# Performance work log

Hardware: AMD Instinct MI355X
Metric: run time of the kernel (lower is better)

The kernel has to match this reference:

```python
import jax, jax.numpy as jnp
import numpy as np

EMBED_DIM = 768
HIDDEN_DIM = 384          # max(embed_dim // 2, 128)
NUM_HEADS = 12
HEAD_DIM = EMBED_DIM // NUM_HEADS
LAYER_VOCAB = 4           # len(target_layers)
THRESHOLD = 0.5
MIN_KEEP_RATIO = 0.1
B, N = 8, 1024


def setup_inputs() -> dict:
    key = jax.random.key(0)
    ks = jax.random.split(key, 12)
    std = 0.02
    return {
        "tokens": jax.random.normal(ks[0], (B, N, EMBED_DIM), jnp.float32),
        "layer_token_idx": 1,
        # actor params
        "layer_emb": jax.random.normal(ks[1], (LAYER_VOCAB, EMBED_DIM), jnp.float32) * std,
        "ln_g": jnp.ones((EMBED_DIM,), jnp.float32),
        "ln_b": jnp.zeros((EMBED_DIM,), jnp.float32),
        "w1": jax.random.normal(ks[2], (HIDDEN_DIM, EMBED_DIM), jnp.float32) * std,
        "b1": jnp.zeros((HIDDEN_DIM,), jnp.float32),
        "w2": jax.random.normal(ks[3], (HIDDEN_DIM, HIDDEN_DIM), jnp.float32) * std,
        "b2": jnp.zeros((HIDDEN_DIM,), jnp.float32),
        "w3": jax.random.normal(ks[4], (1, HIDDEN_DIM), jnp.float32) * std,
        "b3": jnp.zeros((1,), jnp.float32),
        # attention params (timm-style)
        "qkv_w": jax.random.normal(ks[5], (3 * EMBED_DIM, EMBED_DIM), jnp.float32) * std,
        "qkv_b": jnp.zeros((3 * EMBED_DIM,), jnp.float32),
        "proj_w": jax.random.normal(ks[6], (EMBED_DIM, EMBED_DIM), jnp.float32) * std,
        "proj_b": jnp.zeros((EMBED_DIM,), jnp.float32),
    }


def _layernorm(x, g, b, eps=1e-5):
    mu = x.mean(-1, keepdims=True)
    var = ((x - mu) ** 2).mean(-1, keepdims=True)
    return (x - mu) * jax.lax.rsqrt(var + eps) * g + b


def _forward(tokens, layer_token_idx, layer_emb, ln_g, ln_b, w1, b1, w2, b2, w3, b3,
             qkv_w, qkv_b, proj_w, proj_b):
    Bsz, Ntok, C = tokens.shape
    # --- MAPPOActor: logits ---
    ctx = tokens + layer_emb[layer_token_idx]               # broadcast [C]
    ctx = ctx + ctx.mean(axis=1, keepdims=True)             # global context
    h = _layernorm(ctx, ln_g, ln_b)
    h = jax.nn.gelu(h @ w1.T + b1, approximate=False)
    h = jax.nn.gelu(h @ w2.T + b2, approximate=False)
    logits = (h @ w3.T + b3).squeeze(-1)                    # [B, N]
    probs = jax.nn.sigmoid(logits)
    # --- compute_mask: threshold + min-keep topk correction ---
    binary = probs >= THRESHOLD                             # [B, N] bool
    min_keep = max(int(Ntok * MIN_KEEP_RATIO), 1)
    min_keep = min(min_keep, Ntok)
    _, topk_idx = jax.lax.top_k(probs, min_keep)            # [B, min_keep]
    fixed = jnp.zeros((Bsz, Ntok), bool).at[jnp.arange(Bsz)[:, None], topk_idx].set(True)
    need_fix = binary.sum(-1) < min_keep                    # [B]
    mask = jnp.where(need_fix[:, None], fixed, binary)
    mask = mask.at[:, 0].set(True)
    # --- masked attention (timm style) ---
    qkv = tokens @ qkv_w.T + qkv_b                          # [B, N, 3C]
    qkv = qkv.reshape(Bsz, Ntok, 3, NUM_HEADS, HEAD_DIM).transpose(2, 0, 3, 1, 4)
    q, k, v = qkv[0], qkv[1], qkv[2]                        # [B, H, N, D]
    q = q * (HEAD_DIM ** -0.5)
    scores = jnp.einsum("bhnd,bhmd->bhnm", q, k)            # [B, H, N, N]
    neg = jnp.finfo(scores.dtype).min
    scores = jnp.where(mask[:, None, None, :], scores, neg)
    attn = jax.nn.softmax(scores, axis=-1)
    v = v * mask[:, None, :, None].astype(v.dtype)
    out = jnp.einsum("bhnm,bhmd->bhnd", attn, v)
    out = out.transpose(0, 2, 1, 3).reshape(Bsz, Ntok, C)
    out = out @ proj_w.T + proj_b
    out = out * mask[..., None].astype(out.dtype)           # zero_out_queries=True
    return out


def reference(tokens, layer_token_idx, layer_emb, ln_g, ln_b, w1, b1, w2, b2, w3, b3,
              qkv_w, qkv_b, proj_w, proj_b):
    return _forward(tokens, layer_token_idx, layer_emb, ln_g, ln_b, w1, b1, w2, b2,
                    w3, b3, qkv_w, qkv_b, proj_w, proj_b)
```

## Files before the change

kernel.cpp:

```cpp
#include <hip/hip_runtime.h>
#include <cstdint>
#include <cmath>

#define EMBED 768
#define HID 384
#define NHEAD 12
#define HDIM 64
#define BATCH 8
#define NTOK 1024
#define MINKEEP 102

using f32x4  = __attribute__((ext_vector_type(4))) float;
using short8 = __attribute__((ext_vector_type(8))) short;
using short4v = __attribute__((ext_vector_type(4))) short;
using half8  = __attribute__((ext_vector_type(8))) _Float16;

__device__ inline short f2bf(float f) {
  unsigned u = __float_as_uint(f);
  u += 0x7fffu + ((u >> 16) & 1u);
  return (short)(u >> 16);
}
__device__ inline float bf2f(short s) {
  return __uint_as_float(((unsigned)(unsigned short)s) << 16);
}
__device__ inline unsigned pack_bf2(float lo, float hi) {
  unsigned ul = __float_as_uint(lo);
  ul += 0x7fffu + ((ul >> 16) & 1u);
  unsigned uh = __float_as_uint(hi);
  uh += 0x7fffu + ((uh >> 16) & 1u);
  return (ul >> 16) | (uh & 0xffff0000u);
}
__device__ inline void split2h(float v, short& h, short& m) {
  _Float16 h0 = (_Float16)v;
  float r = v - (float)h0;
  _Float16 m0 = (_Float16)r;
  h = __builtin_bit_cast(short, h0);
  m = __builtin_bit_cast(short, m0);
}

__global__ __launch_bounds__(768) void addvec_init_kernel(
    const float* __restrict__ layer_emb, const int* __restrict__ lidx,
    float* __restrict__ addvec) {
  int b = blockIdx.x, c = threadIdx.x;
  addvec[b * EMBED + c] = 2.0f * layer_emb[lidx[0] * EMBED + c];
}

__global__ __launch_bounds__(768) void colmean_kernel(
    const float* __restrict__ tokens, float* __restrict__ addvec) {
  int b = blockIdx.x, chunk = blockIdx.y, c = threadIdx.x;
  const float* tb = tokens + ((size_t)b * NTOK + chunk * 64) * EMBED + c;
  float s = 0.f;
#pragma unroll 8
  for (int n = 0; n < 64; ++n) s += tb[(size_t)n * EMBED];
  atomicAdd(&addvec[b * EMBED + c], s * (1.0f / NTOK));
}

__global__ __launch_bounds__(256) void ln_split_kernel(
    const float* __restrict__ tokens, const float* __restrict__ addvec,
    const float* __restrict__ gamma, const float* __restrict__ beta,
    short* __restrict__ xh, short* __restrict__ xm) {
  int row = blockIdx.x;
  int b = row >> 10;
  __shared__ float s_row[EMBED];
  __shared__ float s_red[4];
  const float* tr = tokens + (size_t)row * EMBED;
  const float* av = addvec + b * EMBED;
  float lsum = 0.f;
  for (int c = threadIdx.x; c < EMBED; c += 256) {
    float v = tr[c] + av[c];
    s_row[c] = v;
    lsum += v;
  }
  for (int o = 32; o; o >>= 1) lsum += __shfl_down(lsum, o, 64);
  int wid = threadIdx.x >> 6;
  if ((threadIdx.x & 63) == 0) s_red[wid] = lsum;
  __syncthreads();
  float mu = (s_red[0] + s_red[1] + s_red[2] + s_red[3]) * (1.f / EMBED);
  float lss = 0.f;
  for (int c = threadIdx.x; c < EMBED; c += 256) {
    float d = s_row[c] - mu;
    lss += d * d;
  }
  for (int o = 32; o; o >>= 1) lss += __shfl_down(lss, o, 64);
  __syncthreads();
  if ((threadIdx.x & 63) == 0) s_red[wid] = lss;
  __syncthreads();
  float var = (s_red[0] + s_red[1] + s_red[2] + s_red[3]) * (1.f / EMBED);
  float rinv = 1.0f / sqrtf(var + 1e-5f);
  for (int c = threadIdx.x; c < EMBED; c += 256) {
    float v = (s_row[c] - mu) * rinv * gamma[c] + beta[c];
    short h, m;
    split2h(v, h, m);
    size_t idx = (size_t)row * EMBED + c;
    xh[idx] = h; xm[idx] = m;
  }
}

__global__ __launch_bounds__(256) void cvt_split2_kernel(
    const float* __restrict__ in, short* __restrict__ oh,
    short* __restrict__ om, int n4) {
  int i = blockIdx.x * 256 + threadIdx.x;
  if (i >= n4) return;
  float4 f = ((const float4*)in)[i];
  short4v h, m;
  short th, tm;
  split2h(f.x, th, tm); h[0] = th; m[0] = tm;
  split2h(f.y, th, tm); h[1] = th; m[1] = tm;
  split2h(f.z, th, tm); h[2] = th; m[2] = tm;
  split2h(f.w, th, tm); h[3] = th; m[3] = tm;
  ((short4v*)oh)[i] = h;
  ((short4v*)om)[i] = m;
}

__device__ inline float gelu_exact(float x) {
  return 0.5f * x * (1.0f + erff(x * 0.70710678118654752f));
}

template <int OUT>
__global__ __launch_bounds__(256) void gemm_split_kernel(
    const short* __restrict__ Ah, const short* __restrict__ Am,
    const short* __restrict__ Wh, const short* __restrict__ Wm,
    const float* __restrict__ bias, short* __restrict__ Ch,
    short* __restrict__ Cm, float* __restrict__ Cf,
    int M, int N, int K) {
  __shared__ short sA[2][64][40];
  __shared__ short sW[2][64][40];
  int tid = threadIdx.x;
  int w = tid >> 6, l = tid & 63, lg = l >> 4, lb = l & 15;
  int wr = (w >> 1) * 32, wc = (w & 1) * 32;
  int row0 = blockIdx.x * 64, col0 = blockIdx.y * 64;
  int srow = tid >> 2;
  int skk = (tid & 3) * 8;
  f32x4 acc0[2][2] = {}, acc1[2][2] = {};
  short8 ra0, ra1, rw0, rw1;
  {
    size_t aoff = (size_t)(row0 + srow) * K + skk;
    size_t woff = (size_t)(col0 + srow) * K + skk;
    ra0 = *(const short8*)(Ah + aoff);
    ra1 = *(const short8*)(Am + aoff);
    rw0 = *(const short8*)(Wh + woff);
    rw1 = *(const short8*)(Wm + woff);
  }
  for (int k0 = 0; k0 < K; k0 += 32) {
    __syncthreads();
    *(short8*)&sA[0][srow][skk] = ra0;
    *(short8*)&sA[1][srow][skk] = ra1;
    *(short8*)&sW[0][srow][skk] = rw0;
    *(short8*)&sW[1][srow][skk] = rw1;
    __syncthreads();
    if (k0 + 32 < K) {
      size_t aoff = (size_t)(row0 + srow) * K + k0 + 32 + skk;
      size_t woff = (size_t)(col0 + srow) * K + k0 + 32 + skk;
      ra0 = *(const short8*)(Ah + aoff);
      ra1 = *(const short8*)(Am + aoff);
      rw0 = *(const short8*)(Wh + woff);
      rw1 = *(const short8*)(Wm + woff);
    }
    half8 ah[2], am[2], bh[2], bm[2];
#pragma unroll
    for (int i = 0; i < 2; ++i) {
      ah[i] = *(half8*)&sA[0][wr + i * 16 + lb][lg * 8];
      am[i] = *(half8*)&sA[1][wr + i * 16 + lb][lg * 8];
      bh[i] = *(half8*)&sW[0][wc + i * 16 + lb][lg * 8];
      bm[i] = *(half8*)&sW[1][wc + i * 16 + lb][lg * 8];
    }
#pragma unroll
    for (int i = 0; i < 2; ++i)
#pragma unroll
      for (int j = 0; j < 2; ++j) {
        f32x4 c0 = acc0[i][j];
        f32x4 c1 = acc1[i][j];
        c0 = __builtin_amdgcn_mfma_f32_16x16x32_f16(ah[i], bh[j], c0, 0, 0, 0);
        c1 = __builtin_amdgcn_mfma_f32_16x16x32_f16(ah[i], bm[j], c1, 0, 0, 0);
        c0 = __builtin_amdgcn_mfma_f32_16x16x32_f16(am[i], bh[j], c0, 0, 0, 0);
        acc0[i][j] = c0;
        acc1[i][j] = c1;
      }
  }
#pragma unroll
  for (int i = 0; i < 2; ++i) {
#pragma unroll
    for (int j = 0; j < 2; ++j) {
#pragma unroll
      for (int r = 0; r < 4; ++r) {
        int grow = row0 + wr + i * 16 + lg * 4 + r;
        int gcol = col0 + wc + j * 16 + lb;
        float g = gelu_exact(acc0[i][j][r] + acc1[i][j][r] + bias[gcol]);
        size_t idx = (size_t)grow * N + gcol;
        if (OUT == 0) {
          short h, m;
          split2h(g, h, m);
          Ch[idx] = h; Cm[idx] = m;
        } else {
          Cf[idx] = g;
        }
      }
    }
  }
}

__global__ __launch_bounds__(256) void logits_kernel(
    const float* __restrict__ h2, const float* __restrict__ w3,
    const float* __restrict__ b3, float* __restrict__ probs) {
  int row = blockIdx.x * 4 + (threadIdx.x >> 6);
  int lane = threadIdx.x & 63;
  const float* hr = h2 + (size_t)row * HID;
  float s = 0.f;
  for (int c = lane; c < HID; c += 64) s += hr[c] * w3[c];
  for (int o = 32; o; o >>= 1) s += __shfl_down(s, o, 64);
  if (lane == 0) probs[row] = 1.0f / (1.0f + expf(-(s + b3[0])));
}

__global__ __launch_bounds__(1024) void mask_kernel(
    const float* __restrict__ probs, int* __restrict__ kidx,
    int* __restrict__ kc, float* __restrict__ biasc) {
  int b = blockIdx.x, tid = threadIdx.x;
  __shared__ unsigned long long keys[1024];
  __shared__ int flag[1024];
  __shared__ int wsum[16];
  float p = probs[b * NTOK + tid];
  bool bin = (p >= 0.5f);
  int wid = tid >> 6, lane = tid & 63;
  unsigned long long bal = __ballot(bin);
  if (lane == 0) wsum[wid] = __popcll(bal);
  __syncthreads();
  int total = 0;
  for (int q = 0; q < 16; ++q) total += wsum[q];
  int mv;
  if (total >= MINKEEP) {
    mv = bin ? 1 : 0;
  } else {
    flag[tid] = 0;
    unsigned u = __float_as_uint(p);
    keys[tid] = ((unsigned long long)u << 32) | (unsigned)(1023 - tid);
    __syncthreads();
    for (int k2 = 2; k2 <= 1024; k2 <<= 1) {
      for (int j = k2 >> 1; j > 0; j >>= 1) {
        int ixj = tid ^ j;
        if (ixj > tid) {
          unsigned long long a = keys[tid], c = keys[ixj];
          bool desc = ((tid & k2) == 0);
          if (desc ? (a < c) : (a > c)) {
            keys[tid] = c;
            keys[ixj] = a;
          }
        }
        __syncthreads();
      }
    }
    if (tid < MINKEEP) {
      int idx = 1023 - (int)(keys[tid] & 0xFFFFFFFFu);
      flag[idx] = 1;
    }
    __syncthreads();
    mv = flag[tid];
  }
  if (tid == 0) mv = 1;
  __syncthreads();
  unsigned long long fb = __ballot(mv != 0);
  if (lane == 0) wsum[wid] = __popcll(fb);
  __syncthreads();
  int base = 0, tot = 0;
  for (int q = 0; q < 16; ++q) {
    int v = wsum[q];
    if (q < wid) base += v;
    tot += v;
  }
  int pre = base + __popcll(fb & ((1ull << lane) - 1ull));
  if (mv) {
    kidx[b * NTOK + pre] = tid;
    biasc[b * NTOK + pre] = 0.f;
  }
  if (tid >= tot) {
    kidx[b * NTOK + tid] = 0;
    biasc[b * NTOK + tid] = -3.0e38f;
  }
  if (tid == 0) kc[b] = tot;
}

__global__ __launch_bounds__(256) void cvt_bf16_kernel(
    const float* __restrict__ in, short* __restrict__ out, int n4) {
  int i = blockIdx.x * 256 + threadIdx.x;
  if (i >= n4) return;
  float4 f = ((const float4*)in)[i];
  short4v s;
  s[0] = f2bf(f.x); s[1] = f2bf(f.y); s[2] = f2bf(f.z); s[3] = f2bf(f.w);
  ((short4v*)out)[i] = s;
}

__global__ __launch_bounds__(256) void qkv_gather_kernel(
    const short* __restrict__ tok_bf, const short* __restrict__ W,
    const float* __restrict__ bias, const int* __restrict__ kidx,
    const int* __restrict__ kc, short* __restrict__ qq,
    short* __restrict__ kk_, short* __restrict__ vv) {
  __shared__ short sA[128][72];
  __shared__ short sW[128][72];
  __shared__ int s_idx[128];
  int bx = blockIdx.x;
  int b = bx & 7, bt = bx >> 3;
  int kcb = kc[b];
  if (bt * 128 >= kcb) return;
  int tid = threadIdx.x;
  if (tid < 128) s_idx[tid] = kidx[b * NTOK + bt * 128 + tid];
  int w = tid >> 6, l = tid & 63, lg = l >> 4, lb = l & 15;
  int wr = (w >> 1) * 64, wc = (w & 1) * 64;
  int col0 = blockIdx.y * 128;
  int r_ = tid >> 3, kq = (tid & 7) * 8;
  __syncthreads();
  const short* Ab = tok_bf + (size_t)b * NTOK * EMBED;
  f32x4 acc[4][4] = {};
  short8 pa[4], pw[4];
#pragma unroll
  for (int t = 0; t < 4; ++t) {
    pa[t] = *(const short8*)(Ab + (size_t)s_idx[t * 32 + r_] * EMBED + kq);
    pw[t] = *(const short8*)(W + (size_t)(col0 + t * 32 + r_) * EMBED + kq);
  }
  for (int k0 = 0; k0 < EMBED; k0 += 64) {
    __syncthreads();
#pragma unroll
    for (int t = 0; t < 4; ++t) {
      *(short8*)&sA[t * 32 + r_][kq] = pa[t];
      *(short8*)&sW[t * 32 + r_][kq] = pw[t];
    }
    __syncthreads();
    if (k0 + 64 < EMBED) {
#pragma unroll
      for (int t = 0; t < 4; ++t) {
        pa[t] = *(const short8*)(Ab + (size_t)s_idx[t * 32 + r_] * EMBED +
                                 k0 + 64 + kq);
        pw[t] = *(const short8*)(W + (size_t)(col0 + t * 32 + r_) * EMBED +
                                 k0 + 64 + kq);
      }
    }
#pragma unroll
    for (int half = 0; half < 2; ++half) {
      short8 af[4], bfr[4];
#pragma unroll
      for (int i = 0; i < 4; ++i)
        af[i] = *(short8*)&sA[wr + i * 16 + lb][half * 32 + lg * 8];
#pragma unroll
      for (int j = 0; j < 4; ++j)
        bfr[j] = *(short8*)&sW[wc + j * 16 + lb][half * 32 + lg * 8];
#pragma unroll
      for (int i = 0; i < 4; ++i)
#pragma unroll
        for (int j = 0; j < 4; ++j)
          acc[i][j] = __builtin_amdgcn_mfma_f32_16x16x32_bf16(af[i], bfr[j],
                                                              acc[i][j], 0, 0, 0);
    }
  }
#pragma unroll
  for (int i = 0; i < 4; ++i) {
#pragma unroll
    for (int j = 0; j < 4; ++j) {
#pragma unroll
      for (int r = 0; r < 4; ++r) {
        int jrow = bt * 128 + wr + i * 16 + lg * 4 + r;
        int gcol = col0 + wc + j * 16 + lb;
        float val = acc[i][j][r] + bias[gcol];
        int which = gcol / EMBED;
        int rem = gcol - which * EMBED;
        int h = rem >> 6, d = rem & 63;
        size_t dst = ((size_t)(b * NHEAD + h) * NTOK + jrow) * HDIM + d;
        if (which == 0)
          qq[dst] = f2bf(val * 0.125f);
        else if (which == 1)
          kk_[dst] = f2bf(val);
        else
          vv[dst] = f2bf(val);
      }
    }
  }
}

__global__ __launch_bounds__(256) void vtrans_kernel(
    const short* __restrict__ Vb, short* __restrict__ VT) {
  int bh = blockIdx.y;
  int n0 = blockIdx.x * 64;
  __shared__ short st[64][72];
  int tid = threadIdx.x;
#pragma unroll
  for (int t = 0; t < 2; ++t) {
    int c = tid + t * 256;
    int n = c >> 3, ds = c & 7;
    *(short8*)&st[n][ds * 8] =
        *(const short8*)(Vb + ((size_t)bh * NTOK + n0 + n) * HDIM + ds * 8);
  }
  __syncthreads();
#pragma unroll
  for (int t = 0; t < 2; ++t) {
    int c = tid + t * 256;
    int d = c >> 3, ns = c & 7;
    short8 tmp;
#pragma unroll
    for (int jj = 0; jj < 8; ++jj) tmp[jj] = st[ns * 8 + jj][d];
    *(short8*)(VT + ((size_t)bh * HDIM + d) * NTOK + n0 + ns * 8) = tmp;
  }
}

#define ATTN_SWZ(row, colbyte) (((row)*128) + ((colbyte) ^ (((row)&7) << 4)))

__global__ __launch_bounds__(256) void attn_mfma3_kernel(
    const short* __restrict__ Qc, const short* __restrict__ Kc,
    const short* __restrict__ VTc, const float* __restrict__ biasc,
    const int* __restrict__ kc, short* __restrict__ ao) {
  __shared__ __align__(16) short sK[64 * 64];
  __shared__ __align__(16) short sVT[64 * 64];
  int bid = blockIdx.x;
  int xcd = bid & 7, slot = bid >> 3;
  int bh = xcd * 12 + (slot >> 3);
  int qt = slot & 7;
  int b = bh / NHEAD;
  int kcb = kc[b];
  if (qt * 128 >= kcb) return;
  int nt = (kcb + 63) >> 6;
  int tid = threadIdx.x;
  int w = tid >> 6, l = tid & 63, lg = l >> 4, lb = l & 15;
  int n0 = qt * 128 + w * 32;
  const short* Qp = Qc + ((size_t)bh * NTOK + n0) * HDIM;
  const short* Kp = Kc + (size_t)bh * NTOK * HDIM;
  const short* Vp = VTc + (size_t)bh * HDIM * NTOK;
  const float* bp = biasc + b * NTOK;

  short8 qf[2][2];
#pragma unroll
  for (int i = 0; i < 2; ++i)
#pragma unroll
    for (int hh = 0; hh < 2; ++hh)
      qf[i][hh] = *(const short8*)(Qp + (i * 16 + lb) * HDIM + hh * 32 + lg * 8);

  f32x4 acc[2][4] = {};
  float lr[2] = {0.f, 0.f};

  int srow = tid >> 3;
  int scol = (tid & 7) * 8;
  int scolb = scol * 2;
  short8 rk0, rk1, rv0, rv1;

#define ATTN_LOADT(m0_)                                                        \
  {                                                                            \
    rk0 = *(const short8*)(Kp + (size_t)((m0_) + srow) * HDIM + scol);         \
    rk1 = *(const short8*)(Kp + (size_t)((m0_) + srow + 32) * HDIM + scol);    \
    rv0 = *(const short8*)(Vp + (size_t)srow * NTOK + (m0_) + scol);           \
    rv1 = *(const short8*)(Vp + (size_t)(srow + 32) * NTOK + (m0_) + scol);    \
  }

  ATTN_LOADT(0);
  for (int t = 0; t < nt; ++t) {
    int m0 = t * 64;
    *(short8*)((char*)sK + ATTN_SWZ(srow, scolb)) = rk0;
    *(short8*)((char*)sK + ATTN_SWZ(srow + 32, scolb)) = rk1;
    *(short8*)((char*)sVT + ATTN_SWZ(srow, scolb)) = rv0;
    *(short8*)((char*)sVT + ATTN_SWZ(srow + 32, scolb)) = rv1;
    __syncthreads();
    if (t + 1 < nt) ATTN_LOADT(m0 + 64);

    f32x4 bias4[4];
#pragma unroll
    for (int s = 0; s < 4; ++s)
      bias4[s] = *(const f32x4*)(bp + m0 + s * 16 + lg * 4);

    f32x4 S[2][4];
#pragma unroll
    for (int s = 0; s < 4; ++s) {
      short8 kf0 = *(const short8*)((const char*)sK +
                                    ATTN_SWZ(s * 16 + lb, lg * 16));
      short8 kf1 = *(const short8*)((const char*)sK +
                                    ATTN_SWZ(s * 16 + lb, 64 + lg * 16));
#pragma unroll
      for (int i = 0; i < 2; ++i) {
        f32x4 c = bias4[s];
        c = __builtin_amdgcn_mfma_f32_16x16x32_bf16(kf0, qf[i][0], c, 0, 0, 0);
        c = __builtin_amdgcn_mfma_f32_16x16x32_bf16(kf1, qf[i][1], c, 0, 0, 0);
        S[i][s] = c;
      }
    }

    unsigned pk[2][4][2];
#pragma unroll
    for (int i = 0; i < 2; ++i) {
      float rs = 0.f;
#pragma unroll
      for (int s = 0; s < 4; ++s) {
        float p0 = __expf(S[i][s][0]);
        float p1 = __expf(S[i][s][1]);
        float p2 = __expf(S[i][s][2]);
        float p3 = __expf(S[i][s][3]);
        rs += (p0 + p1) + (p2 + p3);
        pk[i][s][0] = pack_bf2(p0, p1);
        pk[i][s][1] = pack_bf2(p2, p3);
      }
      rs += __shfl_xor(rs, 16);
      rs += __shfl_xor(rs, 32);
      lr[i] += rs;
    }

    bool hi = (lg & 2) != 0;
    int srcl = ((lg & 1) * 2) * 16 + lb;
#pragma unroll
    for (int t2 = 0; t2 < 2; ++t2) {
      short8 vf[4];
#pragma unroll
      for (int u = 0; u < 4; ++u)
        vf[u] = *(const short8*)((const char*)sVT +
                                 ATTN_SWZ(u * 16 + lb, t2 * 64 + lg * 16));
#pragma unroll
      for (int i = 0; i < 2; ++i) {
        int a0 = __shfl((int)pk[i][2 * t2][0], srcl);
        int b0 = __shfl((int)pk[i][2 * t2 + 1][0], srcl);
        int a1 = __shfl((int)pk[i][2 * t2][1], srcl);
        int b1 = __shfl((int)pk[i][2 * t2 + 1][1], srcl);
        int a2 = __shfl((int)pk[i][2 * t2][0], srcl + 16);
        int b2 = __shfl((int)pk[i][2 * t2 + 1][0], srcl + 16);
        int a3 = __shfl((int)pk[i][2 * t2][1], srcl + 16);
        int b3 = __shfl((int)pk[i][2 * t2 + 1][1], srcl + 16);
        union { short8 s8; int u[4]; } pa;
        pa.u[0] = hi ? b0 : a0;
        pa.u[1] = hi ? b1 : a1;
        pa.u[2] = hi ? b2 : a2;
        pa.u[3] = hi ? b3 : a3;
#pragma unroll
        for (int u = 0; u < 4; ++u)
          acc[i][u] = __builtin_amdgcn_mfma_f32_16x16x32_bf16(pa.s8, vf[u],
                                                              acc[i][u], 0, 0, 0);
      }
    }
    __syncthreads();
  }

  int h = bh - b * NHEAD;
#pragma unroll
  for (int i = 0; i < 2; ++i) {
#pragma unroll
    for (int r = 0; r < 4; ++r) {
      float inv = 1.0f / __shfl(lr[i], lg * 4 + r);
      int j = n0 + i * 16 + lg * 4 + r;
#pragma unroll
      for (int u = 0; u < 4; ++u) {
        ao[((size_t)b * NTOK + j) * EMBED + h * HDIM + u * 16 + lb] =
            f2bf(acc[i][u][r] * inv);
      }
    }
  }
}

__global__ __launch_bounds__(256) void proj_gather_kernel(
    const short* __restrict__ A, const short* __restrict__ W,
    const float* __restrict__ bias, const int* __restrict__ kidx,
    const int* __restrict__ kc, float* __restrict__ out) {
  __shared__ short sA[128][72];
  __shared__ short sW[128][72];
  __shared__ int s_idx[128];
  int bx = blockIdx.x;
  int b = bx & 7, bt = bx >> 3;
  int kcb = kc[b];
  if (bt * 128 >= kcb) return;
  int tid = threadIdx.x;
  if (tid < 128) s_idx[tid] = kidx[b * NTOK + bt * 128 + tid];
  int w = tid >> 6, l = tid & 63, lg = l >> 4, lb = l & 15;
  int wr = (w >> 1) * 64, wc = (w & 1) * 64;
  int col0 = blockIdx.y * 128;
  int r_ = tid >> 3, kq = (tid & 7) * 8;
  const short* Ab = A + ((size_t)b * NTOK + bt * 128) * EMBED;
  f32x4 acc[4][4] = {};
  short8 pa[4], pw[4];
#pragma unroll
  for (int t = 0; t < 4; ++t) {
    pa[t] = *(const short8*)(Ab + (size_t)(t * 32 + r_) * EMBED + kq);
    pw[t] = *(const short8*)(W + (size_t)(col0 + t * 32 + r_) * EMBED + kq);
  }
  for (int k0 = 0; k0 < EMBED; k0 += 64) {
    __syncthreads();
#pragma unroll
    for (int t = 0; t < 4; ++t) {
      *(short8*)&sA[t * 32 + r_][kq] = pa[t];
      *(short8*)&sW[t * 32 + r_][kq] = pw[t];
    }
    __syncthreads();
    if (k0 + 64 < EMBED) {
#pragma unroll
      for (int t = 0; t < 4; ++t) {
        pa[t] = *(const short8*)(Ab + (size_t)(t * 32 + r_) * EMBED + k0 + 64 + kq);
        pw[t] = *(const short8*)(W + (size_t)(col0 + t * 32 + r_) * EMBED + k0 + 64 + kq);
      }
    }
#pragma unroll
    for (int half = 0; half < 2; ++half) {
      short8 af[4], bfr[4];
#pragma unroll
      for (int i = 0; i < 4; ++i)
        af[i] = *(short8*)&sA[wr + i * 16 + lb][half * 32 + lg * 8];
#pragma unroll
      for (int j = 0; j < 4; ++j)
        bfr[j] = *(short8*)&sW[wc + j * 16 + lb][half * 32 + lg * 8];
#pragma unroll
      for (int i = 0; i < 4; ++i)
#pragma unroll
        for (int j = 0; j < 4; ++j)
          acc[i][j] = __builtin_amdgcn_mfma_f32_16x16x32_bf16(af[i], bfr[j],
                                                              acc[i][j], 0, 0, 0);
    }
  }
#pragma unroll
  for (int i = 0; i < 4; ++i) {
#pragma unroll
    for (int j = 0; j < 4; ++j) {
#pragma unroll
      for (int r = 0; r < 4; ++r) {
        int jloc = wr + i * 16 + lg * 4 + r;
        int jrow = bt * 128 + jloc;
        int gcol = col0 + wc + j * 16 + lb;
        if (jrow < kcb) {
          int n = s_idx[jloc];
          out[((size_t)b * NTOK + n) * EMBED + gcol] = acc[i][j][r] + bias[gcol];
        }
      }
    }
  }
}

extern "C" void kernel_launch(void* const* d_in, const int* in_sizes, int n_in,
                              void* d_out, int out_size, void* d_ws, size_t ws_size,
                              hipStream_t stream) {
  const float* tokens   = (const float*)d_in[0];
  const int*   lidx     = (const int*)d_in[1];
  const float* layer_emb= (const float*)d_in[2];
  const float* ln_g     = (const float*)d_in[3];
  const float* ln_b     = (const float*)d_in[4];
  const float* w1       = (const float*)d_in[5];
  const float* b1       = (const float*)d_in[6];
  const float* w2       = (const float*)d_in[7];
  const float* b2       = (const float*)d_in[8];
  const float* w3       = (const float*)d_in[9];
  const float* b3       = (const float*)d_in[10];
  const float* qkv_w    = (const float*)d_in[11];
  const float* qkv_b    = (const float*)d_in[12];
  const float* proj_w   = (const float*)d_in[13];
  const float* proj_b   = (const float*)d_in[14];
  float* out = (float*)d_out;
  float* ws = (float*)d_ws;

  float* addvec = ws;
  float* probs  = ws + 6144;
  int*   kidx   = (int*)(ws + 14336);
  float* biasc  = ws + 22528;
  int*   kc     = (int*)(ws + 30720);
  short* tok_bf = (short*)(ws + 30736);
  short* wq_bf  = (short*)(ws + 3176464);
  short* wp_bf  = (short*)(ws + 4061200);
  short* w1h = (short*)(ws + 4356112);
  short* w1m = (short*)(ws + 4503568);
  short* w2h = (short*)(ws + 4798480);
  short* w2m = (short*)(ws + 4872208);
  const size_t X0 = 5019664;
  short* xh  = (short*)(ws + X0);
  short* xm  = (short*)(ws + X0 + 3145728);
  short* h1h = (short*)(ws + X0 + 9437184);
  short* h1m = (short*)(ws + X0 + 11010048);
  float* h2  = ws + X0 + 14155776;
  short* Qc   = (short*)(ws + X0);
  short* Kc   = (short*)(ws + X0 + 3145728);
  short* Vc   = (short*)(ws + X0 + 6291456);
  short* VTc  = (short*)(ws + X0 + 9437184);
  short* aoc  = (short*)(ws + X0 + 12582912);

  hipMemsetAsync(d_out, 0, (size_t)out_size * sizeof(float), stream);

  cvt_bf16_kernel<<<dim3(6144), dim3(256), 0, stream>>>(tokens, tok_bf, 1572864);
  cvt_bf16_kernel<<<dim3(1728), dim3(256), 0, stream>>>(qkv_w, wq_bf, 442368);
  cvt_bf16_kernel<<<dim3(576),  dim3(256), 0, stream>>>(proj_w, wp_bf, 147456);
  cvt_split2_kernel<<<dim3(288), dim3(256), 0, stream>>>(w1, w1h, w1m, 73728);
  cvt_split2_kernel<<<dim3(144), dim3(256), 0, stream>>>(w2, w2h, w2m, 36864);

  addvec_init_kernel<<<dim3(BATCH), dim3(768), 0, stream>>>(layer_emb, lidx, addvec);
  colmean_kernel<<<dim3(BATCH, 16), dim3(768), 0, stream>>>(tokens, addvec);
  ln_split_kernel<<<dim3(BATCH * NTOK), dim3(256), 0, stream>>>(
      tokens, addvec, ln_g, ln_b, xh, xm);
  gemm_split_kernel<0><<<dim3(128, 6), dim3(256), 0, stream>>>(
      xh, xm, w1h, w1m, b1, h1h, h1m, nullptr,
      BATCH * NTOK, HID, EMBED);
  gemm_split_kernel<1><<<dim3(128, 6), dim3(256), 0, stream>>>(
      h1h, h1m, w2h, w2m, b2, nullptr, nullptr, h2,
      BATCH * NTOK, HID, HID);
  logits_kernel<<<dim3(2048), dim3(256), 0, stream>>>(h2, w3, b3, probs);
  mask_kernel<<<dim3(BATCH), dim3(1024), 0, stream>>>(probs, kidx, kc, biasc);

  qkv_gather_kernel<<<dim3(64, 18), dim3(256), 0, stream>>>(
      tok_bf, wq_bf, qkv_b, kidx, kc, Qc, Kc, Vc);
  vtrans_kernel<<<dim3(16, BATCH * NHEAD), dim3(256), 0, stream>>>(Vc, VTc);
  attn_mfma3_kernel<<<dim3(768), dim3(256), 0, stream>>>(
      Qc, Kc, VTc, biasc, kc, aoc);
  proj_gather_kernel<<<dim3(64, 6), dim3(256), 0, stream>>>(
      aoc, wp_bf, proj_b, kidx, kc, out);
}
```

Measured before the change: 180.8 us.

## Fuse weight conversions, token bf16 cast, and logits head into neighboring kernels

Merges the separate weight-conversion launches and the addvec init into one prep kernel. It folds the token bf16 cast into the layernorm pass so tokens are read once, and fuses the w3 dot product into the second MLP GEMM epilogue using atomics, which removes the h2 buffer and the logits kernel. The mask now thresholds raw logits at zero and sorts an order-preserving float key instead of sigmoid probabilities. This cuts launch count and one full read of tokens and h2, at the cost of adding a memset and atomic contention in the GEMM epilogue.

```diff
diff --git a/kernel.cpp b/kernel.cpp
--- a/kernel.cpp
+++ b/kernel.cpp
@@ -38,11 +38,42 @@
   m = __builtin_bit_cast(short, m0);
 }
 
-__global__ __launch_bounds__(768) void addvec_init_kernel(
+__global__ __launch_bounds__(256) void prep_kernel(
+    const float* __restrict__ qkv_w, short* __restrict__ wq_bf,
+    const float* __restrict__ proj_w, short* __restrict__ wp_bf,
+    const float* __restrict__ w1, short* __restrict__ w1h, short* __restrict__ w1m,
+    const float* __restrict__ w2, short* __restrict__ w2h, short* __restrict__ w2m,
     const float* __restrict__ layer_emb, const int* __restrict__ lidx,
     float* __restrict__ addvec) {
-  int b = blockIdx.x, c = threadIdx.x;
-  addvec[b * EMBED + c] = 2.0f * layer_emb[lidx[0] * EMBED + c];
+  int blk = blockIdx.x, tid = threadIdx.x;
+  if (blk < 2304) {
+    const float* in = (blk < 1728) ? qkv_w : proj_w;
+    short* out = (blk < 1728) ? wq_bf : wp_bf;
+    int i = (blk < 1728 ? blk : blk - 1728) * 256 + tid;
+    float4 f = ((const float4*)in)[i];
+    short4v s;
+    s[0] = f2bf(f.x); s[1] = f2bf(f.y); s[2] = f2bf(f.z); s[3] = f2bf(f.w);
+    ((short4v*)out)[i] = s;
+  } else if (blk < 2736) {
+    const float* in = (blk < 2592) ? w1 : w2;
+    short* oh = (blk < 2592) ? w1h : w2h;
+    short* om = (blk < 2592) ? w1m : w2m;
+    int i = (blk < 2592 ? blk - 2304 : blk - 2592) * 256 + tid;
+    float4 f = ((const float4*)in)[i];
+    short4v h, m;
+    short th, tm;
+    split2h(f.x, th, tm); h[0] = th; m[0] = tm;
+    split2h(f.y, th, tm); h[1] = th; m[1] = tm;
+    split2h(f.z, th, tm); h[2] = th; m[2] = tm;
+    split2h(f.w, th, tm); h[3] = th; m[3] = tm;
+    ((short4v*)oh)[i] = h;
+    ((short4v*)om)[i] = m;
+  } else {
+    int i = (blk - 2736) * 256 + tid;
+    int c = i & (EMBED - 1);
+    c = i % EMBED;
+    addvec[i] = 2.0f * layer_emb[lidx[0] * EMBED + c];
+  }
 }
 
 __global__ __launch_bounds__(768) void colmean_kernel(
@@ -58,7 +89,8 @@
 __global__ __launch_bounds__(256) void ln_split_kernel(
     const float* __restrict__ tokens, const float* __restrict__ addvec,
     const float* __restrict__ gamma, const float* __restrict__ beta,
-    short* __restrict__ xh, short* __restrict__ xm) {
+    short* __restrict__ xh, short* __restrict__ xm,
+    short* __restrict__ tok_bf) {
   int row = blockIdx.x;
   int b = row >> 10;
   __shared__ float s_row[EMBED];
@@ -67,7 +99,9 @@
   const float* av = addvec + b * EMBED;
   float lsum = 0.f;
   for (int c = threadIdx.x; c < EMBED; c += 256) {
-    float v = tr[c] + av[c];
+    float t = tr[c];
+    tok_bf[(size_t)row * EMBED + c] = f2bf(t);
+    float v = t + av[c];
     s_row[c] = v;
     lsum += v;
   }
@@ -96,22 +130,6 @@
   }
 }
 
-__global__ __launch_bounds__(256) void cvt_split2_kernel(
-    const float* __restrict__ in, short* __restrict__ oh,
-    short* __restrict__ om, int n4) {
-  int i = blockIdx.x * 256 + threadIdx.x;
-  if (i >= n4) return;
-  float4 f = ((const float4*)in)[i];
-  short4v h, m;
-  short th, tm;
-  split2h(f.x, th, tm); h[0] = th; m[0] = tm;
-  split2h(f.y, th, tm); h[1] = th; m[1] = tm;
-  split2h(f.z, th, tm); h[2] = th; m[2] = tm;
-  split2h(f.w, th, tm); h[3] = th; m[3] = tm;
-  ((short4v*)oh)[i] = h;
-  ((short4v*)om)[i] = m;
-}
-
 __device__ inline float gelu_exact(float x) {
   return 0.5f * x * (1.0f + erff(x * 0.70710678118654752f));
 }
@@ -121,8 +139,8 @@
     const short* __restrict__ Ah, const short* __restrict__ Am,
     const short* __restrict__ Wh, const short* __restrict__ Wm,
     const float* __restrict__ bias, short* __restrict__ Ch,
-    short* __restrict__ Cm, float* __restrict__ Cf,
-    int M, int N, int K) {
+    short* __restrict__ Cm, const float* __restrict__ w3,
+    float* __restrict__ lgt, int M, int N, int K) {
   __shared__ short sA[2][64][40];
   __shared__ short sW[2][64][40];
   int tid = threadIdx.x;
@@ -177,49 +195,65 @@
         acc1[i][j] = c1;
       }
   }
-#pragma unroll
-  for (int i = 0; i < 2; ++i) {
-#pragma unroll
-    for (int j = 0; j < 2; ++j) {
-#pragma unroll
-      for (int r = 0; r < 4; ++r) {
-        int grow = row0 + wr + i * 16 + lg * 4 + r;
-        int gcol = col0 + wc + j * 16 + lb;
-        float g = gelu_exact(acc0[i][j][r] + acc1[i][j][r] + bias[gcol]);
-        size_t idx = (size_t)grow * N + gcol;
-        if (OUT == 0) {
+  if (OUT == 0) {
+#pragma unroll
+    for (int i = 0; i < 2; ++i) {
+#pragma unroll
+      for (int j = 0; j < 2; ++j) {
+#pragma unroll
+        for (int r = 0; r < 4; ++r) {
+          int grow = row0 + wr + i * 16 + lg * 4 + r;
+          int gcol = col0 + wc + j * 16 + lb;
+          float g = gelu_exact(acc0[i][j][r] + acc1[i][j][r] + bias[gcol]);
+          size_t idx = (size_t)grow * N + gcol;
           short h, m;
           split2h(g, h, m);
           Ch[idx] = h; Cm[idx] = m;
-        } else {
-          Cf[idx] = g;
         }
       }
     }
-  }
-}
-
-__global__ __launch_bounds__(256) void logits_kernel(
-    const float* __restrict__ h2, const float* __restrict__ w3,
-    const float* __restrict__ b3, float* __restrict__ probs) {
-  int row = blockIdx.x * 4 + (threadIdx.x >> 6);
-  int lane = threadIdx.x & 63;
-  const float* hr = h2 + (size_t)row * HID;
-  float s = 0.f;
-  for (int c = lane; c < HID; c += 64) s += hr[c] * w3[c];
-  for (int o = 32; o; o >>= 1) s += __shfl_down(s, o, 64);
-  if (lane == 0) probs[row] = 1.0f / (1.0f + expf(-(s + b3[0])));
+  } else {
+    float part[2][4];
+#pragma unroll
+    for (int i = 0; i < 2; ++i)
+#pragma unroll
+      for (int r = 0; r < 4; ++r) part[i][r] = 0.f;
+#pragma unroll
+    for (int i = 0; i < 2; ++i) {
+#pragma unroll
+      for (int j = 0; j < 2; ++j) {
+#pragma unroll
+        for (int r = 0; r < 4; ++r) {
+          int gcol = col0 + wc + j * 16 + lb;
+          float g = gelu_exact(acc0[i][j][r] + acc1[i][j][r] + bias[gcol]);
+          part[i][r] += g * w3[gcol];
+        }
+      }
+    }
+#pragma unroll
+    for (int i = 0; i < 2; ++i) {
+#pragma unroll
+      for (int r = 0; r < 4; ++r) {
+        float v = part[i][r];
+        v += __shfl_xor(v, 1);
+        v += __shfl_xor(v, 2);
+        v += __shfl_xor(v, 4);
+        v += __shfl_xor(v, 8);
+        if (lb == 0) atomicAdd(&lgt[row0 + wr + i * 16 + lg * 4 + r], v);
+      }
+    }
+  }
 }
 
 __global__ __launch_bounds__(1024) void mask_kernel(
-    const float* __restrict__ probs, int* __restrict__ kidx,
-    int* __restrict__ kc, float* __restrict__ biasc) {
+    const float* __restrict__ lgt, const float* __restrict__ b3,
+    int* __restrict__ kidx, int* __restrict__ kc, float* __restrict__ biasc) {
   int b = blockIdx.x, tid = threadIdx.x;
   __shared__ unsigned long long keys[1024];
   __shared__ int flag[1024];
   __shared__ int wsum[16];
-  float p = probs[b * NTOK + tid];
-  bool bin = (p >= 0.5f);
+  float v = lgt[b * NTOK + tid] + b3[0];
+  bool bin = (v >= 0.0f);
   int wid = tid >> 6, lane = tid & 63;
   unsigned long long bal = __ballot(bin);
   if (lane == 0) wsum[wid] = __popcll(bal);
@@ -231,7 +265,8 @@
     mv = bin ? 1 : 0;
   } else {
     flag[tid] = 0;
-    unsigned u = __float_as_uint(p);
+    unsigned u = __float_as_uint(v);
+    u = (u & 0x80000000u) ? ~u : (u | 0x80000000u);
     keys[tid] = ((unsigned long long)u << 32) | (unsigned)(1023 - tid);
     __syncthreads();
     for (int k2 = 2; k2 <= 1024; k2 <<= 1) {
@@ -262,9 +297,9 @@
   __syncthreads();
   int base = 0, tot = 0;
   for (int q = 0; q < 16; ++q) {
-    int v = wsum[q];
-    if (q < wid) base += v;
-    tot += v;
+    int vq = wsum[q];
+    if (q < wid) base += vq;
+    tot += vq;
   }
   int pre = base + __popcll(fb & ((1ull << lane) - 1ull));
   if (mv) {
@@ -276,16 +311,6 @@
     biasc[b * NTOK + tid] = -3.0e38f;
   }
   if (tid == 0) kc[b] = tot;
-}
-
-__global__ __launch_bounds__(256) void cvt_bf16_kernel(
-    const float* __restrict__ in, short* __restrict__ out, int n4) {
-  int i = blockIdx.x * 256 + threadIdx.x;
-  if (i >= n4) return;
-  float4 f = ((const float4*)in)[i];
-  short4v s;
-  s[0] = f2bf(f.x); s[1] = f2bf(f.y); s[2] = f2bf(f.z); s[3] = f2bf(f.w);
-  ((short4v*)out)[i] = s;
 }
 
 __global__ __launch_bounds__(256) void qkv_gather_kernel(
@@ -641,7 +666,7 @@
   float* ws = (float*)d_ws;
 
   float* addvec = ws;
-  float* probs  = ws + 6144;
+  float* lgt    = ws + 6144;
   int*   kidx   = (int*)(ws + 14336);
   float* biasc  = ws + 22528;
   int*   kc     = (int*)(ws + 30720);
@@ -657,7 +682,6 @@
   short* xm  = (short*)(ws + X0 + 3145728);
   short* h1h = (short*)(ws + X0 + 9437184);
   short* h1m = (short*)(ws + X0 + 11010048);
-  float* h2  = ws + X0 + 14155776;
   short* Qc   = (short*)(ws + X0);
   short* Kc   = (short*)(ws + X0 + 3145728);
   short* Vc   = (short*)(ws + X0 + 6291456);
@@ -665,25 +689,22 @@
   short* aoc  = (short*)(ws + X0 + 12582912);
 
   hipMemsetAsync(d_out, 0, (size_t)out_size * sizeof(float), stream);
-
-  cvt_bf16_kernel<<<dim3(6144), dim3(256), 0, stream>>>(tokens, tok_bf, 1572864);
-  cvt_bf16_kernel<<<dim3(1728), dim3(256), 0, stream>>>(qkv_w, wq_bf, 442368);
-  cvt_bf16_kernel<<<dim3(576),  dim3(256), 0, stream>>>(proj_w, wp_bf, 147456);
-  cvt_split2_kernel<<<dim3(288), dim3(256), 0, stream>>>(w1, w1h, w1m, 73728);
-  cvt_split2_kernel<<<dim3(144), dim3(256), 0, stream>>>(w2, w2h, w2m, 36864);
-
-  addvec_init_kernel<<<dim3(BATCH), dim3(768), 0, stream>>>(layer_emb, lidx, addvec);
+  hipMemsetAsync(lgt, 0, BATCH * NTOK * sizeof(float), stream);
+
+  prep_kernel<<<dim3(2760), dim3(256), 0, stream>>>(
+      qkv_w, wq_bf, proj_w, wp_bf, w1, w1h, w1m, w2, w2h, w2m,
+      layer_emb, lidx, addvec);
+
   colmean_kernel<<<dim3(BATCH, 16), dim3(768), 0, stream>>>(tokens, addvec);
   ln_split_kernel<<<dim3(BATCH * NTOK), dim3(256), 0, stream>>>(
-      tokens, addvec, ln_g, ln_b, xh, xm);
+      tokens, addvec, ln_g, ln_b, xh, xm, tok_bf);
   gemm_split_kernel<0><<<dim3(128, 6), dim3(256), 0, stream>>>(
-      xh, xm, w1h, w1m, b1, h1h, h1m, nullptr,
+      xh, xm, w1h, w1m, b1, h1h, h1m, nullptr, nullptr,
       BATCH * NTOK, HID, EMBED);
   gemm_split_kernel<1><<<dim3(128, 6), dim3(256), 0, stream>>>(
-      h1h, h1m, w2h, w2m, b2, nullptr, nullptr, h2,
+      h1h, h1m, w2h, w2m, b2, nullptr, nullptr, w3, lgt,
       BATCH * NTOK, HID, HID);
-  logits_kernel<<<dim3(2048), dim3(256), 0, stream>>>(h2, w3, b3, probs);
-  mask_kernel<<<dim3(BATCH), dim3(1024), 0, stream>>>(probs, kidx, kc, biasc);
+  mask_kernel<<<dim3(BATCH), dim3(1024), 0, stream>>>(lgt, b3, kidx, kc, biasc);
 
   qkv_gather_kernel<<<dim3(64, 18), dim3(256), 0, stream>>>(
       tok_bf, wq_bf, qkv_b, kidx, kc, Qc, Kc, Vc);
```

Result: faster. 166.4 us (-8.0%).
